# Optimization experiments

Measured on AMD Instinct MI355X. Metric: run time of the kernel, lower is better.

The kernel has to match this reference:

```python
import jax, jax.numpy as jnp
import numpy as np

G = 4  # number of groups


def _group_vals(h, shift, Ua, Ua1, Ua2, Ua3):
    # h: [B, H]; Ua: [g, H/g, r]; Ua1/2/3: [g, r, H/g]
    B, H = h.shape
    hg = h.reshape(B, G, H // G)
    if shift:
        # torch index = rotate-left by `shift`: new group j reads old group (j+shift)%g
        hg = jnp.roll(hg, -shift, axis=1)
    t = jnp.einsum('bgd,gdr->bgr', hg, Ua)  # shared low-rank projection
    proj = lambda M: jnp.einsum('bgr,grd->bgd', t, M).reshape(B, H)
    return proj(Ua1), proj(Ua2), proj(Ua3)


def setup_inputs() -> dict:
    key = jax.random.key(0)
    ks = jax.random.split(key, 24)
    B, I, H, wR = 8192, 1024, 1024, 256
    hg = H // G
    r01, r23 = 64, 32
    d = {}
    d['x'] = jax.random.normal(ks[0], (B, I), dtype=jnp.float32)
    d['h'] = jax.random.normal(ks[1], (B, H), dtype=jnp.float32)
    d['W'] = 0.1 * jax.random.normal(ks[2], (I, wR), dtype=jnp.float32)
    d['W1'] = 0.1 * jax.random.normal(ks[3], (wR, H), dtype=jnp.float32)
    d['W2'] = 0.1 * jax.random.normal(ks[4], (wR, H), dtype=jnp.float32)
    d['W3'] = 0.1 * jax.random.normal(ks[5], (wR, H), dtype=jnp.float32)
    d['U'] = 0.1 * jax.random.normal(ks[6], (G, hg, r01), dtype=jnp.float32)
    d['U1'] = 0.1 * jax.random.normal(ks[7], (G, r01, hg), dtype=jnp.float32)
    d['U2'] = 0.1 * jax.random.normal(ks[8], (G, r01, hg), dtype=jnp.float32)
    d['U3'] = 0.1 * jax.random.normal(ks[9], (G, r01, hg), dtype=jnp.float32)
    d['UU'] = 0.1 * jax.random.normal(ks[10], (G, hg, r01), dtype=jnp.float32)
    d['UU1'] = 0.1 * jax.random.normal(ks[11], (G, r01, hg), dtype=jnp.float32)
    d['UU2'] = 0.1 * jax.random.normal(ks[12], (G, r01, hg), dtype=jnp.float32)
    d['UU3'] = 0.1 * jax.random.normal(ks[13], (G, r01, hg), dtype=jnp.float32)
    d['UUU'] = 0.1 * jax.random.normal(ks[14], (G, hg, r23), dtype=jnp.float32)
    d['UUU1'] = 0.1 * jax.random.normal(ks[15], (G, r23, hg), dtype=jnp.float32)
    d['UUU2'] = 0.1 * jax.random.normal(ks[16], (G, r23, hg), dtype=jnp.float32)
    d['UUU3'] = 0.1 * jax.random.normal(ks[17], (G, r23, hg), dtype=jnp.float32)
    d['UUUU'] = 0.1 * jax.random.normal(ks[18], (G, hg, r23), dtype=jnp.float32)
    d['UUUU1'] = 0.1 * jax.random.normal(ks[19], (G, r23, hg), dtype=jnp.float32)
    d['UUUU2'] = 0.1 * jax.random.normal(ks[20], (G, r23, hg), dtype=jnp.float32)
    d['UUUU3'] = 0.1 * jax.random.normal(ks[21], (G, r23, hg), dtype=jnp.float32)
    d['bias_r'] = jnp.ones((1, H), dtype=jnp.float32)
    d['bias_gate'] = jnp.ones((1, H), dtype=jnp.float32)
    d['bias_update'] = jnp.ones((1, H), dtype=jnp.float32)
    return d


def reference(x, h, W, W1, W2, W3, U, U1, U2, U3, UU, UU1, UU2, UU3,
              UUU, UUU1, UUU2, UUU3, UUUU, UUUU1, UUUU2, UUUU3,
              bias_r, bias_gate, bias_update):
    u1, u2, u3 = _group_vals(h, 0, U, U1, U2, U3)
    uu1, uu2, uu3 = _group_vals(h, 1, UU, UU1, UU2, UU3)
    uuu1, uuu2, uuu3 = _group_vals(h, 2, UUU, UUU1, UUU2, UUU3)
    uuuu1, uuuu2, uuuu3 = _group_vals(h, 3, UUUU, UUUU1, UUUU2, UUUU3)
    xw = x @ W  # [B, wRank]
    w1, w2, w3 = xw @ W1, xw @ W2, xw @ W3
    r = jax.nn.sigmoid(w1 + u1 + uu1 + uuu1 + uuuu1 + bias_r)
    z = jax.nn.sigmoid(w2 + u2 + uu2 + uuu2 + uuuu2 + bias_gate)
    c_tilda = jnp.tanh(w3 + r * (u3 + uu3 + uuu3 + uuuu3) + bias_update)
    return z * h + (1.0 - z) * c_tilda
```

## Files before the change

kernel.cpp:

```cpp
#include <hip/hip_runtime.h>

typedef short bf16x8 __attribute__((ext_vector_type(8)));
typedef float f32x4 __attribute__((ext_vector_type(4)));
typedef float f32x16 __attribute__((ext_vector_type(16)));

__device__ __forceinline__ unsigned short f2bf(float f) {
  union { float f; unsigned u; } c; c.f = f;
  unsigned u = c.u;
  u += 0x7FFFu + ((u >> 16) & 1u);
  return (unsigned short)(u >> 16);
}
__device__ __forceinline__ float bf2f(unsigned short h) {
  union { unsigned u; float f; } c; c.u = ((unsigned)h) << 16;
  return c.f;
}
__device__ __forceinline__ void split2(float v, unsigned short& hi, unsigned short& lo) {
  union { float f; unsigned u; } c; c.f = v;
  unsigned uh = c.u & 0xFFFF0000u;
  hi = (unsigned short)(uh >> 16);
  union { unsigned u; float f; } d; d.u = uh;
  lo = f2bf(v - d.f);
}
__device__ __forceinline__ void gload16(const void* g, void* l) {
  __builtin_amdgcn_global_load_lds((const __attribute__((address_space(1))) void*)g,
                                   (__attribute__((address_space(3))) void*)l, 16, 0, 0);
}
__device__ __forceinline__ float sigm(float x) { return 1.0f / (1.0f + __expf(-x)); }
__device__ __forceinline__ float tanha(float x) { return 1.0f - 2.0f / (1.0f + __expf(2.0f * x)); }

__global__ __launch_bounds__(256) void s123(
    const float* __restrict__ W,
    const float* __restrict__ U, const float* __restrict__ UU,
    const float* __restrict__ UUU, const float* __restrict__ UUUU,
    const float* __restrict__ W1, const float* __restrict__ W2, const float* __restrict__ W3,
    const float* __restrict__ A1, const float* __restrict__ A2, const float* __restrict__ A3,
    const float* __restrict__ B1, const float* __restrict__ B2, const float* __restrict__ B3,
    const float* __restrict__ C1, const float* __restrict__ C2, const float* __restrict__ C3,
    const float* __restrict__ D1, const float* __restrict__ D2, const float* __restrict__ D3,
    unsigned short* __restrict__ Wt, unsigned short* __restrict__ Bg,
    unsigned short* __restrict__ Btp) {
  int gidx = blockIdx.x * 256 + threadIdx.x;
  if (gidx < 262144) {
    int k = gidx >> 8, n = gidx & 255;
    Wt[n * 1024 + k] = f2bf(W[gidx]);
  } else if (gidx < 458752) {
    int idx = gidx - 262144;
    int g = idx / 49152;
    int rem = idx - g * 49152;
    int k = rem / 192, n = rem - k * 192;
    int jj = 0, rr = n;
#pragma unroll
    for (int s = 0; s < 3; ++s) {
      int w = (((g - jj) & 3) < 2) ? 64 : 32;
      if (rr >= w) { rr -= w; ++jj; }
    }
    int v = (g - jj) & 3;
    int rv = (v < 2) ? 64 : 32;
    const float* M = (v == 0) ? U : (v == 1) ? UU : (v == 2) ? UUU : UUUU;
    Bg[g * 49152 + n * 256 + k] = f2bf(M[(jj * 256 + k) * rv + rr]);
  } else {
    int idx = gidx - 458752;
    int c  = idx & 255;
    int t1 = idx >> 8;
    int k2 = t1 & 63;
    int t2 = t1 >> 6;
    int q  = t2 % 3;
    int t3 = t2 / 3;
    int j  = t3 / 11, kt = t3 - (t3 / 11) * 11;
    float val;
    if (kt < 8) {
      int kk = (kt * 64 + k2) & 255;
      const float* Wp = (q == 0) ? W1 : (q == 1) ? W2 : W3;
      val = Wp[kk * 1024 + j * 256 + c];
    } else {
      int kT = (kt - 8) * 64 + k2;
      int v, r, rv;
      if (kT < 64)       { v = 0; r = kT;       rv = 64; }
      else if (kT < 128) { v = 1; r = kT - 64;  rv = 64; }
      else if (kT < 160) { v = 2; r = kT - 128; rv = 32; }
      else               { v = 3; r = kT - 160; rv = 32; }
      const float* M;
      if (v == 0)      M = (q == 0) ? A1 : (q == 1) ? A2 : A3;
      else if (v == 1) M = (q == 0) ? B1 : (q == 1) ? B2 : B3;
      else if (v == 2) M = (q == 0) ? C1 : (q == 1) ? C2 : C3;
      else             M = (q == 0) ? D1 : (q == 1) ? D2 : D3;
      val = M[(j * rv + r) * 256 + c];
    }
    Btp[j * 540672 + kt * 49152 + (c >> 4) * 3072 + q * 1024 + (c & 15) * 64 + k2] = f2bf(val);
  }
}

__global__ __launch_bounds__(256) void g1_xw(const float* __restrict__ x,
                                             const unsigned short* __restrict__ Wt,
                                             unsigned short* __restrict__ Abuf) {
  __shared__ char lds[49152];
  const int tid = threadIdx.x, lane = tid & 63, wid = tid >> 6;
  const int nb = blockIdx.x, mb = blockIdx.y;
  const int wn = wid;
  f32x4 acc[2][2] = {};
  float4 xr[2];
  const int r0 = tid >> 4, f4c = tid & 15;
  const float* xbase = x + (size_t)(mb * 32) * 1024 + f4c * 4;

  auto loadX = [&](int kt) {
#pragma unroll
    for (int q = 0; q < 2; ++q)
      xr[q] = *(const float4*)(xbase + (size_t)(q * 16 + r0) * 1024 + kt * 64);
  };
  auto writeA = [&](int buf) {
#pragma unroll
    for (int q = 0; q < 2; ++q) {
      int row = q * 16 + r0;
      float4 v = xr[q];
      unsigned short h0, h1, h2, h3, l0, l1, l2, l3;
      split2(v.x, h0, l0); split2(v.y, h1, l1);
      split2(v.z, h2, l2); split2(v.w, h3, l3);
      int ba = row * 128 + ((f4c * 8) ^ ((row & 7) << 4));
      *(uint2*)(lds + buf * 4096 + ba) =
          make_uint2(((unsigned)h1 << 16) | h0, ((unsigned)h3 << 16) | h2);
      *(uint2*)(lds + 8192 + buf * 4096 + ba) =
          make_uint2(((unsigned)l1 << 16) | l0, ((unsigned)l3 << 16) | l2);
    }
  };
  auto stageB = [&](int kt, int buf) {
#pragma unroll
    for (int it = 0; it < 4; ++it) {
      int nloc = it * 32 + wid * 8 + (lane >> 3);
      const char* src = (const char*)Wt + (size_t)(nb * 128 + nloc) * 2048 + kt * 128
                        + (((lane & 7) * 16) ^ ((nloc & 7) << 4));
      gload16(src, lds + 16384 + buf * 16384 + (it * 32 + wid * 8) * 128);
    }
  };

  loadX(0); stageB(0, 0); writeA(0);
  __syncthreads();
#pragma unroll 2
  for (int kt = 0; kt < 16; ++kt) {
    int buf = kt & 1;
    if (kt < 15) {
      loadX(kt + 1); stageB(kt + 1, buf ^ 1);
      asm volatile("s_waitcnt vmcnt(6)" ::: "memory");
    } else {
      asm volatile("s_waitcnt vmcnt(0)" ::: "memory");
    }
    __builtin_amdgcn_s_barrier();
    __builtin_amdgcn_sched_barrier(0);
    const char* hA = lds + buf * 4096;
    const char* lA = lds + 8192 + buf * 4096;
    const char* bB = lds + 16384 + buf * 16384;
#pragma unroll
    for (int ks = 0; ks < 2; ++ks) {
      bf16x8 ah[2], al[2], b[2];
#pragma unroll
      for (int mf = 0; mf < 2; ++mf) {
        int mloc = mf * 16 + (lane & 15);
        int ka = (ks * 64 + (lane >> 4) * 16) ^ ((mloc & 7) << 4);
        ah[mf] = *(const bf16x8*)(hA + mloc * 128 + ka);
        al[mf] = *(const bf16x8*)(lA + mloc * 128 + ka);
      }
#pragma unroll
      for (int nf = 0; nf < 2; ++nf) {
        int nloc = wn * 32 + nf * 16 + (lane & 15);
        int kb = (ks * 64 + (lane >> 4) * 16) ^ ((nloc & 7) << 4);
        b[nf] = *(const bf16x8*)(bB + nloc * 128 + kb);
      }
#pragma unroll
      for (int mf = 0; mf < 2; ++mf)
#pragma unroll
        for (int nf = 0; nf < 2; ++nf) {
          acc[mf][nf] = __builtin_amdgcn_mfma_f32_16x16x32_bf16(ah[mf], b[nf], acc[mf][nf], 0, 0, 0);
          acc[mf][nf] = __builtin_amdgcn_mfma_f32_16x16x32_bf16(al[mf], b[nf], acc[mf][nf], 0, 0, 0);
        }
    }
    if (kt < 15) writeA(buf ^ 1);
    __builtin_amdgcn_sched_barrier(0);
    asm volatile("s_waitcnt lgkmcnt(0)" ::: "memory");
    __builtin_amdgcn_s_barrier();
  }
#pragma unroll
  for (int mf = 0; mf < 2; ++mf)
#pragma unroll
    for (int nf = 0; nf < 2; ++nf)
#pragma unroll
      for (int r = 0; r < 4; ++r) {
        int row = mb * 32 + mf * 16 + (lane >> 4) * 4 + r;
        int col = nb * 128 + wn * 32 + nf * 16 + (lane & 15);
        float val = acc[mf][nf][r];
        unsigned short hi, lo;
        split2(val, hi, lo);
        Abuf[(size_t)row * 1280 + col] = hi;
        Abuf[(size_t)row * 1280 + 256 + col] = lo;
      }
}

__global__ __launch_bounds__(256) void g2_t(const float* __restrict__ h,
                                            const unsigned short* __restrict__ Bg,
                                            unsigned short* __restrict__ Abuf) {
  __shared__ char lds[65536];
  const int tid = threadIdx.x, lane = tid & 63, wid = tid >> 6;
  const int mb = blockIdx.x, g = blockIdx.y;
  const int wm = wid >> 1, wn = wid & 1;
  f32x4 acc[2][6] = {};
  float4 hr[4];
  const int r0 = tid >> 4, f4c = tid & 15;
  const float* hbase = h + (size_t)(mb * 64) * 1024 + g * 256 + f4c * 4;

  auto loadH = [&](int kt) {
#pragma unroll
    for (int q = 0; q < 4; ++q)
      hr[q] = *(const float4*)(hbase + (size_t)(q * 16 + r0) * 1024 + kt * 64);
  };
  auto writeA = [&](int buf) {
#pragma unroll
    for (int q = 0; q < 4; ++q) {
      int row = q * 16 + r0;
      float4 v = hr[q];
      int ba = row * 128 + ((f4c * 8) ^ ((row & 7) << 4));
      *(uint2*)(lds + buf * 8192 + ba) =
          make_uint2(((unsigned)f2bf(v.y) << 16) | f2bf(v.x),
                     ((unsigned)f2bf(v.w) << 16) | f2bf(v.z));
    }
  };
  auto stageB = [&](int kt, int buf) {
#pragma unroll
    for (int it = 0; it < 6; ++it) {
      int nloc = it * 32 + wid * 8 + (lane >> 3);
      const char* src = (const char*)Bg + (size_t)(g * 192 + nloc) * 512 + kt * 128
                        + (((lane & 7) * 16) ^ ((nloc & 7) << 4));
      gload16(src, lds + 16384 + buf * 24576 + (it * 32 + wid * 8) * 128);
    }
  };

  loadH(0); stageB(0, 0); writeA(0);
  __syncthreads();
#pragma unroll
  for (int kt = 0; kt < 4; ++kt) {
    int buf = kt & 1;
    if (kt < 3) { loadH(kt + 1); stageB(kt + 1, buf ^ 1); }
    const char* cA = lds + buf * 8192;
    const char* cB = lds + 16384 + buf * 24576;
#pragma unroll
    for (int ks = 0; ks < 2; ++ks) {
      bf16x8 a[2], b[6];
#pragma unroll
      for (int mf = 0; mf < 2; ++mf) {
        int mloc = wm * 32 + mf * 16 + (lane & 15);
        int ka = (ks * 64 + (lane >> 4) * 16) ^ ((mloc & 7) << 4);
        a[mf] = *(const bf16x8*)(cA + mloc * 128 + ka);
      }
#pragma unroll
      for (int nf = 0; nf < 6; ++nf) {
        int nloc = wn * 96 + nf * 16 + (lane & 15);
        int kb = (ks * 64 + (lane >> 4) * 16) ^ ((nloc & 7) << 4);
        b[nf] = *(const bf16x8*)(cB + nloc * 128 + kb);
      }
#pragma unroll
      for (int mf = 0; mf < 2; ++mf)
#pragma unroll
        for (int nf = 0; nf < 6; ++nf)
          acc[mf][nf] = __builtin_amdgcn_mfma_f32_16x16x32_bf16(a[mf], b[nf], acc[mf][nf], 0, 0, 0);
    }
    if (kt < 3) writeA(buf ^ 1);
    __syncthreads();
  }
#pragma unroll
  for (int mf = 0; mf < 2; ++mf)
#pragma unroll
    for (int nf = 0; nf < 6; ++nf) {
      int n = wn * 96 + nf * 16 + (lane & 15);
      int jj = 0, rr = n;
#pragma unroll
      for (int s = 0; s < 3; ++s) {
        int w = (((g - jj) & 3) < 2) ? 64 : 32;
        if (rr >= w) { rr -= w; ++jj; }
      }
      int v = (g - jj) & 3;
      int offv = (v < 2) ? (v << 6) : (64 + (v << 5));
      int col = 512 + jj * 192 + offv + rr;
#pragma unroll
      for (int r = 0; r < 4; ++r) {
        int row = mb * 64 + wm * 32 + mf * 16 + (lane >> 4) * 4 + r;
        Abuf[(size_t)row * 1280 + col] = f2bf(acc[mf][nf][r]);
      }
    }
}

__global__ __launch_bounds__(256) void g3_main(const unsigned short* __restrict__ Abuf,
                                               const unsigned short* __restrict__ Btp,
                                               const float* __restrict__ h,
                                               const float* __restrict__ bias_r,
                                               const float* __restrict__ bias_g,
                                               const float* __restrict__ bias_u,
                                               float* __restrict__ out) {
  __shared__ char lds[81920];
  const int tid = threadIdx.x, lane = tid & 63, wid = tid >> 6;
  const int cb = blockIdx.x & 3, j = blockIdx.x >> 2;
  const int mb = blockIdx.y;
  const int wm = wid >> 1, wn = wid & 1;
  f32x16 acc[2][4] = {};

  const char* AbufB = (const char*)Abuf + (size_t)mb * 128 * 2560;
  const char* BtpJ  = (const char*)Btp + (size_t)j * 1081344;
  int thrA[4], dstA[4], thrB[6], dstB[6];
#pragma unroll
  for (int it = 0; it < 4; ++it) {
    int mloc = wid * 32 + it * 8 + (lane >> 3);
    thrA[it] = mloc * 2560 + (((lane & 7) * 16) ^ ((mloc & 7) << 4));
    dstA[it] = (wid * 32 + it * 8) * 128;
  }
#pragma unroll
  for (int it = 0; it < 6; ++it) {
    int rB = it * 32 + wid * 8 + (lane >> 3);
    thrB[it] = rB * 128 + (((lane & 7) * 16) ^ ((rB & 7) << 4));
    dstB[it] = (it * 32 + wid * 8) * 128;
  }
  int pA[2][4], pB[3][4];
#pragma unroll
  for (int mblk = 0; mblk < 2; ++mblk) {
    int row = wm * 64 + mblk * 32 + (lane & 31);
#pragma unroll
    for (int k4 = 0; k4 < 4; ++k4)
      pA[mblk][k4] = row * 128 + ((k4 * 32 + ((lane >> 5) << 4)) ^ ((row & 7) << 4));
  }
#pragma unroll
  for (int q = 0; q < 3; ++q) {
    int rB = ((wn * 2 + ((lane >> 4) & 1)) * 3 + q) * 16 + (lane & 15);
#pragma unroll
    for (int k4 = 0; k4 < 4; ++k4)
      pB[q][k4] = 32768 + rB * 128 + ((k4 * 32 + ((lane >> 5) << 4)) ^ ((rB & 7) << 4));
  }

  auto stage = [&](int kt, int buf) {
    int colb2 = (kt < 8) ? kt * 128 : (1024 + j * 384 + (kt - 8) * 128);
#pragma unroll
    for (int it = 0; it < 4; ++it)
      gload16(AbufB + colb2 + thrA[it], lds + buf * 16384 + dstA[it]);
    const char* bsrc = BtpJ + (size_t)(kt * 16 + cb * 4) * 6144;
#pragma unroll
    for (int it = 0; it < 6; ++it)
      gload16(bsrc + thrB[it], lds + 32768 + buf * 24576 + dstB[it]);
  };

  stage(0, 0);
#pragma unroll
  for (int kt = 0; kt < 11; ++kt) {
    const int buf = kt & 1;
    if (kt < 10) {
      stage(kt + 1, buf ^ 1);
      asm volatile("s_waitcnt vmcnt(10)" ::: "memory");
    } else {
      asm volatile("s_waitcnt vmcnt(0)" ::: "memory");
    }
    __builtin_amdgcn_s_barrier();
    __builtin_amdgcn_sched_barrier(0);
    __builtin_amdgcn_s_setprio(1);
#pragma unroll
    for (int k4 = 0; k4 < 4; ++k4) {
      bf16x8 a0 = *(const bf16x8*)(lds + buf * 16384 + pA[0][k4]);
      bf16x8 a1 = *(const bf16x8*)(lds + buf * 16384 + pA[1][k4]);
#pragma unroll
      for (int q = 0; q < 3; ++q) {
        const int p = (kt < 8) ? q : ((q == 2) ? 3 : q);
        bf16x8 b = *(const bf16x8*)(lds + buf * 24576 + pB[q][k4]);
        acc[0][p] = __builtin_amdgcn_mfma_f32_32x32x16_bf16(a0, b, acc[0][p], 0, 0, 0);
        acc[1][p] = __builtin_amdgcn_mfma_f32_32x32x16_bf16(a1, b, acc[1][p], 0, 0, 0);
      }
    }
    __builtin_amdgcn_s_setprio(0);
    __builtin_amdgcn_sched_barrier(0);
    __builtin_amdgcn_s_barrier();
  }
  int cg = j * 256 + cb * 64 + wn * 32 + (lane & 31);
  float br = bias_r[cg], bg = bias_g[cg], bu = bias_u[cg];
#pragma unroll
  for (int mblk = 0; mblk < 2; ++mblk)
#pragma unroll
    for (int r = 0; r < 16; ++r) {
      int row = mb * 128 + wm * 64 + mblk * 32 + (r & 3) + 8 * (r >> 2) + 4 * (lane >> 5);
      float p0 = acc[mblk][0][r], p1 = acc[mblk][1][r];
      float p2 = acc[mblk][2][r], p3 = acc[mblk][3][r];
      float rr = sigm(p0 + br);
      float zz = sigm(p1 + bg);
      float ct = tanha(p2 + rr * p3 + bu);
      float hv = h[(size_t)row * 1024 + cg];
      out[(size_t)row * 1024 + cg] = zz * hv + (1.0f - zz) * ct;
    }
}

extern "C" void kernel_launch(void* const* d_in, const int* in_sizes, int n_in,
                              void* d_out, int out_size, void* d_ws, size_t ws_size,
                              hipStream_t stream) {
  const float* x   = (const float*)d_in[0];
  const float* h   = (const float*)d_in[1];
  const float* W   = (const float*)d_in[2];
  const float* W1  = (const float*)d_in[3];
  const float* W2  = (const float*)d_in[4];
  const float* W3  = (const float*)d_in[5];
  const float* U   = (const float*)d_in[6];
  const float* U1  = (const float*)d_in[7];
  const float* U2  = (const float*)d_in[8];
  const float* U3  = (const float*)d_in[9];
  const float* UU   = (const float*)d_in[10];
  const float* UU1  = (const float*)d_in[11];
  const float* UU2  = (const float*)d_in[12];
  const float* UU3  = (const float*)d_in[13];
  const float* UUU   = (const float*)d_in[14];
  const float* UUU1  = (const float*)d_in[15];
  const float* UUU2  = (const float*)d_in[16];
  const float* UUU3  = (const float*)d_in[17];
  const float* UUUU   = (const float*)d_in[18];
  const float* UUUU1  = (const float*)d_in[19];
  const float* UUUU2  = (const float*)d_in[20];
  const float* UUUU3  = (const float*)d_in[21];
  const float* bias_r = (const float*)d_in[22];
  const float* bias_g = (const float*)d_in[23];
  const float* bias_u = (const float*)d_in[24];

  char* ws = (char*)d_ws;
  unsigned short* Abuf = (unsigned short*)(ws);
  unsigned short* Wt   = (unsigned short*)(ws + 20971520);
  unsigned short* Bg   = (unsigned short*)(ws + 21495808);
  unsigned short* Btp  = (unsigned short*)(ws + 21889024);
  float* out = (float*)d_out;

  s123<<<10240, 256, 0, stream>>>(W, U, UU, UUU, UUUU,
                                  W1, W2, W3, U1, U2, U3, UU1, UU2, UU3,
                                  UUU1, UUU2, UUU3, UUUU1, UUUU2, UUUU3,
                                  Wt, Bg, Btp);
  g1_xw<<<dim3(2, 256), 256, 0, stream>>>(x, Wt, Abuf);
  g2_t<<<dim3(128, 4), 256, 0, stream>>>(h, Bg, Abuf);
  g3_main<<<dim3(16, 64), 256, 0, stream>>>(Abuf, Btp, h, bias_r, bias_g, bias_u, out);
}
```

Measured before the change: 105.8 us.

## Store GEMM operands in MFMA fragment order for contiguous LDS staging

```diff
diff --git a/kernel.cpp b/kernel.cpp
--- a/kernel.cpp
+++ b/kernel.cpp
@@ -27,6 +27,12 @@
 }
 __device__ __forceinline__ float sigm(float x) { return 1.0f / (1.0f + __expf(-x)); }
 __device__ __forceinline__ float tanha(float x) { return 1.0f - 2.0f / (1.0f + __expf(2.0f * x)); }
+
+__device__ __forceinline__ size_t fragIdxA(int row, int col) {
+  int mb = row >> 7, rb = (row >> 5) & 3, l5 = row & 31;
+  int cc = col >> 6, k4 = (col >> 4) & 3, hi = (col >> 3) & 1, e = col & 7;
+  return ((size_t)(mb * 20 + cc) * 16 + rb * 4 + k4) * 512 + (hi * 32 + l5) * 8 + e;
+}
 
 __global__ __launch_bounds__(256) void s123(
     const float* __restrict__ W,
@@ -41,13 +47,14 @@
     unsigned short* __restrict__ Btp) {
   int gidx = blockIdx.x * 256 + threadIdx.x;
   if (gidx < 262144) {
-    int k = gidx >> 8, n = gidx & 255;
-    Wt[n * 1024 + k] = f2bf(W[gidx]);
+    int idx = gidx;
+    int n = idx >> 10, k = idx & 1023;
+    Wt[idx] = f2bf(W[k * 256 + n]);
   } else if (gidx < 458752) {
     int idx = gidx - 262144;
     int g = idx / 49152;
     int rem = idx - g * 49152;
-    int k = rem / 192, n = rem - k * 192;
+    int n = rem >> 8, k = rem & 255;
     int jj = 0, rr = n;
 #pragma unroll
     for (int s = 0; s < 3; ++s) {
@@ -57,16 +64,17 @@
     int v = (g - jj) & 3;
     int rv = (v < 2) ? 64 : 32;
     const float* M = (v == 0) ? U : (v == 1) ? UU : (v == 2) ? UUU : UUUU;
-    Bg[g * 49152 + n * 256 + k] = f2bf(M[(jj * 256 + k) * rv + rr]);
+    Bg[idx] = f2bf(M[(jj * 256 + k) * rv + rr]);
   } else {
     int idx = gidx - 458752;
-    int c  = idx & 255;
-    int t1 = idx >> 8;
-    int k2 = t1 & 63;
-    int t2 = t1 >> 6;
-    int q  = t2 % 3;
-    int t3 = t2 / 3;
-    int j  = t3 / 11, kt = t3 - (t3 / 11) * 11;
+    int blk = idx / 12288;
+    int w   = idx - blk * 12288;
+    int frag = w >> 9, fl = (w >> 3) & 63, e = w & 7;
+    int cb = blk & 3, jk = blk >> 2;
+    int kt = jk % 11, j = jk / 11;
+    int q = frag >> 3, colblk = (frag >> 2) & 1, k4 = frag & 3;
+    int c  = cb * 64 + colblk * 32 + (fl & 31);
+    int k2 = k4 * 16 + (fl >> 5) * 8 + e;
     float val;
     if (kt < 8) {
       int kk = (kt * 64 + k2) & 255;
@@ -86,7 +94,7 @@
       else             M = (q == 0) ? D1 : (q == 1) ? D2 : D3;
       val = M[(j * rv + r) * 256 + c];
     }
-    Btp[j * 540672 + kt * 49152 + (c >> 4) * 3072 + q * 1024 + (c & 15) * 64 + k2] = f2bf(val);
+    Btp[idx] = f2bf(val);
   }
 }
 
@@ -95,7 +103,7 @@
                                              unsigned short* __restrict__ Abuf) {
   __shared__ char lds[49152];
   const int tid = threadIdx.x, lane = tid & 63, wid = tid >> 6;
-  const int nb = blockIdx.x, mb = blockIdx.y;
+  const int mb = blockIdx.x, nb = blockIdx.y;
   const int wn = wid;
   f32x4 acc[2][2] = {};
   float4 xr[2];
@@ -188,8 +196,8 @@
         float val = acc[mf][nf][r];
         unsigned short hi, lo;
         split2(val, hi, lo);
-        Abuf[(size_t)row * 1280 + col] = hi;
-        Abuf[(size_t)row * 1280 + 256 + col] = lo;
+        Abuf[fragIdxA(row, col)] = hi;
+        Abuf[fragIdxA(row, col + 256)] = lo;
       }
 }
 
@@ -280,7 +288,7 @@
 #pragma unroll
       for (int r = 0; r < 4; ++r) {
         int row = mb * 64 + wm * 32 + mf * 16 + (lane >> 4) * 4 + r;
-        Abuf[(size_t)row * 1280 + col] = f2bf(acc[mf][nf][r]);
+        Abuf[fragIdxA(row, col)] = f2bf(acc[mf][nf][r]);
       }
     }
 }
@@ -294,51 +302,23 @@
                                                float* __restrict__ out) {
   __shared__ char lds[81920];
   const int tid = threadIdx.x, lane = tid & 63, wid = tid >> 6;
-  const int cb = blockIdx.x & 3, j = blockIdx.x >> 2;
-  const int mb = blockIdx.y;
+  const int mb = blockIdx.x, cb = blockIdx.y, j = blockIdx.z;
   const int wm = wid >> 1, wn = wid & 1;
   f32x16 acc[2][4] = {};
 
-  const char* AbufB = (const char*)Abuf + (size_t)mb * 128 * 2560;
-  const char* BtpJ  = (const char*)Btp + (size_t)j * 1081344;
-  int thrA[4], dstA[4], thrB[6], dstB[6];
-#pragma unroll
-  for (int it = 0; it < 4; ++it) {
-    int mloc = wid * 32 + it * 8 + (lane >> 3);
-    thrA[it] = mloc * 2560 + (((lane & 7) * 16) ^ ((mloc & 7) << 4));
-    dstA[it] = (wid * 32 + it * 8) * 128;
-  }
-#pragma unroll
-  for (int it = 0; it < 6; ++it) {
-    int rB = it * 32 + wid * 8 + (lane >> 3);
-    thrB[it] = rB * 128 + (((lane & 7) * 16) ^ ((rB & 7) << 4));
-    dstB[it] = (it * 32 + wid * 8) * 128;
-  }
-  int pA[2][4], pB[3][4];
-#pragma unroll
-  for (int mblk = 0; mblk < 2; ++mblk) {
-    int row = wm * 64 + mblk * 32 + (lane & 31);
-#pragma unroll
-    for (int k4 = 0; k4 < 4; ++k4)
-      pA[mblk][k4] = row * 128 + ((k4 * 32 + ((lane >> 5) << 4)) ^ ((row & 7) << 4));
-  }
-#pragma unroll
-  for (int q = 0; q < 3; ++q) {
-    int rB = ((wn * 2 + ((lane >> 4) & 1)) * 3 + q) * 16 + (lane & 15);
-#pragma unroll
-    for (int k4 = 0; k4 < 4; ++k4)
-      pB[q][k4] = 32768 + rB * 128 + ((k4 * 32 + ((lane >> 5) << 4)) ^ ((rB & 7) << 4));
-  }
+  const char* AbufB = (const char*)Abuf;
+  const char* BtpB  = (const char*)Btp;
 
   auto stage = [&](int kt, int buf) {
-    int colb2 = (kt < 8) ? kt * 128 : (1024 + j * 384 + (kt - 8) * 128);
+    int cc = (kt < 8) ? kt : (8 + j * 3 + (kt - 8));
+    const char* asrc = AbufB + (size_t)(mb * 20 + cc) * 16384 + tid * 16;
+    const char* bsrc = BtpB + (size_t)(((j * 11 + kt) * 4 + cb)) * 24576 + tid * 16;
 #pragma unroll
     for (int it = 0; it < 4; ++it)
-      gload16(AbufB + colb2 + thrA[it], lds + buf * 16384 + dstA[it]);
-    const char* bsrc = BtpJ + (size_t)(kt * 16 + cb * 4) * 6144;
+      gload16(asrc + it * 4096, lds + buf * 16384 + it * 4096 + wid * 1024);
 #pragma unroll
     for (int it = 0; it < 6; ++it)
-      gload16(bsrc + thrB[it], lds + 32768 + buf * 24576 + dstB[it]);
+      gload16(bsrc + it * 4096, lds + 32768 + buf * 24576 + it * 4096 + wid * 1024);
   };
 
   stage(0, 0);
@@ -354,14 +334,16 @@
     __builtin_amdgcn_s_barrier();
     __builtin_amdgcn_sched_barrier(0);
     __builtin_amdgcn_s_setprio(1);
+    const char* aB = lds + buf * 16384 + wm * 8192 + lane * 16;
+    const char* bB = lds + 32768 + buf * 24576 + wn * 4096 + lane * 16;
 #pragma unroll
     for (int k4 = 0; k4 < 4; ++k4) {
-      bf16x8 a0 = *(const bf16x8*)(lds + buf * 16384 + pA[0][k4]);
-      bf16x8 a1 = *(const bf16x8*)(lds + buf * 16384 + pA[1][k4]);
+      bf16x8 a0 = *(const bf16x8*)(aB + k4 * 1024);
+      bf16x8 a1 = *(const bf16x8*)(aB + 4096 + k4 * 1024);
 #pragma unroll
       for (int q = 0; q < 3; ++q) {
         const int p = (kt < 8) ? q : ((q == 2) ? 3 : q);
-        bf16x8 b = *(const bf16x8*)(lds + buf * 24576 + pB[q][k4]);
+        bf16x8 b = *(const bf16x8*)(bB + q * 8192 + k4 * 1024);
         acc[0][p] = __builtin_amdgcn_mfma_f32_32x32x16_bf16(a0, b, acc[0][p], 0, 0, 0);
         acc[1][p] = __builtin_amdgcn_mfma_f32_32x32x16_bf16(a1, b, acc[1][p], 0, 0, 0);
       }
@@ -427,7 +409,7 @@
                                   W1, W2, W3, U1, U2, U3, UU1, UU2, UU3,
                                   UUU1, UUU2, UUU3, UUUU1, UUUU2, UUUU3,
                                   Wt, Bg, Btp);
-  g1_xw<<<dim3(2, 256), 256, 0, stream>>>(x, Wt, Abuf);
+  g1_xw<<<dim3(256, 2), 256, 0, stream>>>(x, Wt, Abuf);
   g2_t<<<dim3(128, 4), 256, 0, stream>>>(h, Bg, Abuf);
-  g3_main<<<dim3(16, 64), 256, 0, stream>>>(Abuf, Btp, h, bias_r, bias_g, bias_u, out);
-}
+  g3_main<<<dim3(64, 4, 4), 256, 0, stream>>>(Abuf, Btp, h, bias_r, bias_g, bias_u, out);
+}
```

Result: faster. 94.70 us (-10.5%).
